# Kernel tuning notes

Hardware: AMD Instinct MI355X
Metric: run time of the kernel (lower is better)

The kernel has to match this reference:

```python
import math
import jax, jax.numpy as jnp
import numpy as np

D_MODEL = 1024
N_HEADS = 16
HEAD_DIM = D_MODEL // N_HEADS
WINDOW = 1024
BATCH = 2
SEQ = 2048


def _alibi_slopes(n_heads):
    # power-of-2 branch of ALiBiPositionalEmbedding._get_slopes
    start = 2 ** (-2 ** (-(math.log2(n_heads) - 3)))
    return jnp.asarray([start * start ** i for i in range(n_heads)], dtype=jnp.float32)


def setup_inputs() -> dict:
    key = jax.random.key(0)
    ks = jax.random.split(key, 5)
    scale = 0.02
    return {
        "x": jax.random.normal(ks[0], (BATCH, SEQ, D_MODEL), dtype=jnp.float32),
        "wq": jax.random.normal(ks[1], (D_MODEL, D_MODEL), dtype=jnp.float32) * scale,
        "bq": jnp.zeros((D_MODEL,), dtype=jnp.float32),
        "wk": jax.random.normal(ks[2], (D_MODEL, D_MODEL), dtype=jnp.float32) * scale,
        "bk": jnp.zeros((D_MODEL,), dtype=jnp.float32),
        "wv": jax.random.normal(ks[3], (D_MODEL, D_MODEL), dtype=jnp.float32) * scale,
        "bv": jnp.zeros((D_MODEL,), dtype=jnp.float32),
        "wo": jax.random.normal(ks[4], (D_MODEL, D_MODEL), dtype=jnp.float32) * scale,
        "bo": jnp.zeros((D_MODEL,), dtype=jnp.float32),
    }


def reference(x, wq, bq, wk, bk, wv, bv, wo, bo):
    B, S, _ = x.shape
    # projections (torch Linear: y = x @ W.T + b)
    q = (x @ wq.T + bq).reshape(B, S, N_HEADS, HEAD_DIM).transpose(0, 2, 1, 3)
    k = (x @ wk.T + bk).reshape(B, S, N_HEADS, HEAD_DIM).transpose(0, 2, 1, 3)
    v = (x @ wv.T + bv).reshape(B, S, N_HEADS, HEAD_DIM).transpose(0, 2, 1, 3)

    scores = jnp.einsum("bhqd,bhkd->bhqk", q, k) / math.sqrt(HEAD_DIM)

    # ALiBi bias: -|i-j| * slope_h, shape [H, S, S]
    pos = jnp.arange(S)
    slopes = _alibi_slopes(N_HEADS)  # [H]
    pos_diff = -jnp.abs(pos[None, :] - pos[:, None]).astype(scores.dtype)  # [S,S]
    scores = scores + pos_diff[None, None, :, :] * slopes[None, :, None, None]

    # causal + sliding-window mask: allow row-WINDOW < col <= row
    row = pos[:, None]
    col = pos[None, :]
    mask = (col > row) | (col <= row - WINDOW)  # [S,S] True = masked out
    neg = jnp.finfo(scores.dtype).min
    scores = jnp.where(mask[None, None, :, :], neg, scores)

    probs = jax.nn.softmax(scores, axis=-1)
    out = jnp.einsum("bhqk,bhkd->bhqd", probs, v)  # [B,H,S,D]
    out = out.transpose(0, 2, 1, 3).reshape(B, S, D_MODEL)
    return out @ wo.T + bo
```

## Files before the change

kernel.cpp:

```cpp
#include <hip/hip_runtime.h>
#include <cstdint>
#include <cstddef>

#define S_LEN 2048
#define NH 16
#define HD 64
#define DM 1024
#define WIN 1024

typedef unsigned short u16;
typedef __attribute__((ext_vector_type(8))) short bf16x8;
typedef __attribute__((ext_vector_type(4))) short bf16x4;
typedef __attribute__((ext_vector_type(4))) float f32x4;
typedef __attribute__((ext_vector_type(4))) u16 u16x4;
typedef __attribute__((ext_vector_type(2))) uint32_t u32x2;
typedef __attribute__((ext_vector_type(4))) uint32_t u32x4;

__device__ inline u16 f2b(float f) {
  union { float f; uint32_t u; } x; x.f = f;
  uint32_t r = x.u + 0x7FFFu + ((x.u >> 16) & 1u);
  return (u16)(r >> 16);
}

__device__ inline uint32_t cvt_pk_bf16(float a, float b) {
  uint32_t r;
  asm("v_cvt_pk_bf16_f32 %0, %1, %2" : "=v"(r) : "v"(a), "v"(b));
  return r;
}

__device__ inline void gload16(const void* g, void* l) {
  __builtin_amdgcn_global_load_lds((const __attribute__((address_space(1))) void*)g,
                                   (__attribute__((address_space(3))) void*)l, 16, 0, 0);
}

__global__ __launch_bounds__(256) void cvt_kernel(const float* __restrict__ src,
                                                  u16* __restrict__ dst, int n) {
  int i = (blockIdx.x * 256 + threadIdx.x) * 4;
  if (i >= n) return;
  f32x4 v = *(const f32x4*)(src + i);
  u16x4 o;
  o[0] = f2b(v[0]); o[1] = f2b(v[1]); o[2] = f2b(v[2]); o[3] = f2b(v[3]);
  *(u16x4*)(dst + i) = o;
}

__global__ __launch_bounds__(256)
void cvt4_kernel(const float* __restrict__ a, const float* __restrict__ b,
                 const float* __restrict__ c, const float* __restrict__ d,
                 u16* __restrict__ oa, u16* __restrict__ ob,
                 u16* __restrict__ oc, u16* __restrict__ od) {
  const float* src; u16* dst;
  switch (blockIdx.y) {
    case 0: src = a; dst = oa; break;
    case 1: src = b; dst = ob; break;
    case 2: src = c; dst = oc; break;
    default: src = d; dst = od; break;
  }
  int i = (blockIdx.x * 256 + threadIdx.x) * 4;
  f32x4 v = *(const f32x4*)(src + i);
  u16x4 o;
  o[0] = f2b(v[0]); o[1] = f2b(v[1]); o[2] = f2b(v[2]); o[3] = f2b(v[3]);
  *(u16x4*)(dst + i) = o;
}

template<int EPI>
__global__ __launch_bounds__(256, 4)
void gemm_nt(const u16* __restrict__ A, const u16* __restrict__ B,
             const float* __restrict__ b0, const float* __restrict__ b1,
             const float* __restrict__ b2,
             float* __restrict__ outF, u16* __restrict__ outQ,
             int M, int N, int K) {
  __shared__ u16 As[128 * 32];
  __shared__ u16 Bs[128 * 32];
  const int t = threadIdx.x;
  const int lane = t & 63, wid = t >> 6;
  const int l15 = lane & 15, l4 = lane >> 4;
  const int wr = wid >> 1, wc = wid & 1;
  const int bmB = M >> 7, bnB = N >> 7;
  const int stripe = bmB >> 3;
  const int per = stripe * bnB;
  const int job = (blockIdx.x & 7) * per + (blockIdx.x >> 3);
  const int r_ = job % per;
  const int bm = ((job / per) * stripe + r_ / bnB) << 7;
  const int bn = (r_ % bnB) << 7;
  const int srow = wid * 16 + (lane >> 2), scol = (lane & 3) * 8;
  const u16* Ag = A + (size_t)(bm + srow) * K + scol;
  const u16* Bg = B + (size_t)(bn + srow) * K + scol;
  u16* As0 = As + wid * 512;
  u16* As1 = As + 2048 + wid * 512;
  u16* Bs0 = Bs + wid * 512;
  u16* Bs1 = Bs + 2048 + wid * 512;
  const size_t rstep = (size_t)64 * K;
  f32x4 acc[4][4];
#pragma unroll
  for (int i = 0; i < 4; i++)
#pragma unroll
    for (int j = 0; j < 4; j++) acc[i][j] = (f32x4){0.f, 0.f, 0.f, 0.f};

  for (int kb = 0; kb < K; kb += 32) {
    __syncthreads();
    gload16(Ag + kb, As0);
    gload16(Ag + kb + rstep, As1);
    gload16(Bg + kb, Bs0);
    gload16(Bg + kb + rstep, Bs1);
    __syncthreads();
    bf16x8 af[4], bq[4];
#pragma unroll
    for (int mi = 0; mi < 4; mi++)
      af[mi] = *(bf16x8*)&As[(wr * 64 + mi * 16 + l15) * 32 + l4 * 8];
#pragma unroll
    for (int ni = 0; ni < 4; ni++)
      bq[ni] = *(bf16x8*)&Bs[(wc * 64 + ni * 16 + l15) * 32 + l4 * 8];
#pragma unroll
    for (int mi = 0; mi < 4; mi++)
#pragma unroll
      for (int ni = 0; ni < 4; ni++)
        acc[mi][ni] = __builtin_amdgcn_mfma_f32_16x16x32_bf16(af[mi], bq[ni], acc[mi][ni], 0, 0, 0);
  }

  const int cb = bn >> 10;
  const float* bp = (EPI == 0) ? b0 : (cb == 0 ? b0 : (cb == 1 ? b1 : b2));
#pragma unroll
  for (int mi = 0; mi < 4; mi++) {
#pragma unroll
    for (int ni = 0; ni < 4; ni++) {
#pragma unroll
      for (int r = 0; r < 4; r++) {
        int row = bm + wr * 64 + mi * 16 + l4 * 4 + r;
        int col = bn + wc * 64 + ni * 16 + l15;
        float v = acc[mi][ni][r] + bp[col & (DM - 1)];
        if (EPI == 0) {
          outF[(size_t)row * N + col] = v;
        } else {
          int b = row >> 11, s = row & (S_LEN - 1);
          int which = col >> 10, cw = col & (DM - 1);
          int h = cw >> 6, d = cw & (HD - 1);
          outQ[(size_t)which * 4194304 +
               (((size_t)(b * NH + h)) * S_LEN + s) * HD + d] = f2b(v);
        }
      }
    }
  }
}

__global__ __launch_bounds__(256)
void transpose_v(const u16* __restrict__ V, u16* __restrict__ Vt) {
  const int bh = blockIdx.y;
  const int s0 = blockIdx.x * 64;
  __shared__ u16 tile[64][72];
  const int t = threadIdx.x;
  const u16* src = V + ((size_t)bh * S_LEN + s0) * HD;
#pragma unroll
  for (int i = 0; i < 2; i++) {
    int e = t * 8 + i * 2048;
    int r = e >> 6, c = e & 63;
    *(bf16x8*)&tile[r][c] = *(const bf16x8*)(src + e);
  }
  __syncthreads();
  u16* dst = Vt + (size_t)bh * HD * S_LEN + s0;
#pragma unroll
  for (int i = 0; i < 2; i++) {
    int e = t * 8 + i * 2048;
    int d = e >> 6, s = e & 63;
    bf16x8 tmp;
#pragma unroll
    for (int j = 0; j < 8; j++) tmp[j] = (short)tile[s + j][d];
    *(bf16x8*)&dst[(size_t)d * S_LEN + s] = tmp;
  }
}

__device__ __forceinline__ void stage_tiles(const char* __restrict__ Kg,
                                            const char* __restrict__ Vg,
                                            u16* __restrict__ Kl, u16* __restrict__ Vl,
                                            int t) {
#pragma unroll
  for (int shot = 0; shot < 2; shot++) {
    int o = shot * 4096 + t * 16;
    int sw = ((o >> 7) & 7) << 4;
    gload16(Kg + (o ^ sw), (char*)Kl + o);
    gload16(Vg + (size_t)(o >> 7) * 4096 + ((o & 127) ^ sw), (char*)Vl + o);
  }
}

__device__ __forceinline__ void process_tile16(
    int kb, const u16* __restrict__ Kl, const u16* __restrict__ Vl,
    const bf16x8 qf[2], const float c16[16],
    int qw, int l15, int hi, float slope2, float qks,
    float& m, float& lsum, f32x4 O[4]) {
  const int x = l15 & 7;
  f32x4 st[4];
#pragma unroll
  for (int f = 0; f < 4; f++) st[f] = (f32x4){0.f, 0.f, 0.f, 0.f};
#pragma unroll
  for (int ks = 0; ks < 2; ks++)
#pragma unroll
    for (int f = 0; f < 4; f++) {
      bf16x8 kf = *(const bf16x8*)&Kl[(16 * f + l15) * 64 + (((4 * ks + hi) ^ x) << 3)];
      st[f] = __builtin_amdgcn_mfma_f32_16x16x32_bf16(kf, qf[ks], st[f], 0, 0, 0);
    }

  const int dkb = kb + 4 * hi - (qw + l15);
  const float base = slope2 * (float)dkb;
  const bool interior = (kb + 63 <= qw) && (kb - (qw + 15) > -WIN);
  float p[16];
  if (interior) {
#pragma unroll
    for (int f = 0; f < 4; f++)
#pragma unroll
      for (int r = 0; r < 4; r++)
        p[4 * f + r] = fmaf(st[f][r], qks, base + c16[4 * f + r]);
  } else {
#pragma unroll
    for (int f = 0; f < 4; f++)
#pragma unroll
      for (int r = 0; r < 4; r++) {
        int dk = dkb + 16 * f + r;
        float s = fmaf(st[f][r], qks, base + c16[4 * f + r]);
        p[4 * f + r] = (dk > 0 || dk <= -WIN) ? -3e38f : s;
      }
  }

  float t8[8];
#pragma unroll
  for (int r = 0; r < 8; r++) t8[r] = fmaxf(p[r], p[r + 8]);
#pragma unroll
  for (int r = 0; r < 4; r++) t8[r] = fmaxf(t8[r], t8[r + 4]);
  float rmax = fmaxf(fmaxf(t8[0], t8[1]), fmaxf(t8[2], t8[3]));
  rmax = fmaxf(rmax, __shfl_xor(rmax, 16, 64));
  rmax = fmaxf(rmax, __shfl_xor(rmax, 32, 64));

  if (!__all(rmax <= m + 8.f)) {
    float mn = fmaxf(m, rmax);
    float sc = exp2f(m - mn);
    m = mn;
    lsum *= sc;
#pragma unroll
    for (int d = 0; d < 4; d++)
#pragma unroll
      for (int r = 0; r < 4; r++) O[d][r] *= sc;
  }

#pragma unroll
  for (int r = 0; r < 16; r++) p[r] = exp2f(p[r] - m);
  float a8[8];
#pragma unroll
  for (int r = 0; r < 8; r++) a8[r] = p[r] + p[r + 8];
#pragma unroll
  for (int r = 0; r < 4; r++) a8[r] += a8[r + 4];
  lsum += (a8[0] + a8[1]) + (a8[2] + a8[3]);

  bf16x8 pb[2];
#pragma unroll
  for (int kc = 0; kc < 2; kc++) {
    u32x4 w4;
    w4[0] = cvt_pk_bf16(p[8 * kc + 0], p[8 * kc + 1]);
    w4[1] = cvt_pk_bf16(p[8 * kc + 2], p[8 * kc + 3]);
    w4[2] = cvt_pk_bf16(p[8 * kc + 4], p[8 * kc + 5]);
    w4[3] = cvt_pk_bf16(p[8 * kc + 6], p[8 * kc + 7]);
    pb[kc] = __builtin_bit_cast(bf16x8, w4);
  }

#pragma unroll
  for (int d = 0; d < 4; d++) {
#pragma unroll
    for (int kc = 0; kc < 2; kc++) {
      const int row = (16 * d + l15) * 64;
      bf16x4 a = *(const bf16x4*)&Vl[row + (((4 * kc + (hi >> 1)) ^ x) << 3) + 4 * (hi & 1)];
      bf16x4 bql = *(const bf16x4*)&Vl[row + (((4 * kc + 2 + (hi >> 1)) ^ x) << 3) + 4 * (hi & 1)];
      bf16x8 vf;
      vf[0] = a[0]; vf[1] = a[1]; vf[2] = a[2]; vf[3] = a[3];
      vf[4] = bql[0]; vf[5] = bql[1]; vf[6] = bql[2]; vf[7] = bql[3];
      O[d] = __builtin_amdgcn_mfma_f32_16x16x32_bf16(vf, pb[kc], O[d], 0, 0, 0);
    }
  }
}

__global__ __launch_bounds__(256, 4)
void attn_kernel(const u16* __restrict__ Q, const u16* __restrict__ Kg,
                 const u16* __restrict__ Vt, u16* __restrict__ attn) {
  __shared__ __align__(16) u16 Klds[2][4096];
  __shared__ __align__(16) u16 Vlds[2][4096];
  const int bid = blockIdx.x;
  const int job = (bid & 7) * 128 + (bid >> 3);
  const int bh = job >> 5;
  const int qb = ((31 - (job & 31)) + (bh << 3)) & 31;
  const int b = bh >> 4, h = bh & 15;
  const int tid = threadIdx.x;
  const int wid = tid >> 6, lane = tid & 63;
  const int l15 = lane & 15, hi = lane >> 4;
  const int q0 = qb << 6;
  const int qw = q0 + 16 * wid;
  const u16* Qp = Q + (size_t)bh * (S_LEN * HD);
  const char* Kbase = (const char*)(Kg + (size_t)bh * (S_LEN * HD));
  const char* Vbase = (const char*)(Vt + (size_t)bh * (HD * S_LEN));

  bf16x8 qf[2];
#pragma unroll
  for (int ks = 0; ks < 2; ks++)
    qf[ks] = *(const bf16x8*)(Qp + (size_t)(qw + l15) * HD + 32 * ks + 8 * hi);

  const float slope2 = exp2f(-0.5f * (float)(h + 1)) * 1.44269504f;
  const float qks = 0.125f * 1.44269504f;
  float c16[16];
#pragma unroll
  for (int f = 0; f < 4; f++)
#pragma unroll
    for (int r = 0; r < 4; r++) c16[4 * f + r] = slope2 * (float)(16 * f + r);

  float m = -1e30f, lsum = 0.f;
  f32x4 O[4];
#pragma unroll
  for (int d = 0; d < 4; d++) O[d] = (f32x4){0.f, 0.f, 0.f, 0.f};

  int lo_u = q0 - (WIN - 1); if (lo_u < 0) lo_u = 0; lo_u &= ~63;
  const int hi_u = q0;
  int lo_w = qw - (WIN - 1); if (lo_w < 0) lo_w = 0; lo_w &= ~63;
  const int last_w = (qw + 15) & ~63;

  stage_tiles(Kbase + (size_t)lo_u * 128, Vbase + (size_t)lo_u * 2,
              Klds[0], Vlds[0], tid);
  int cur = 0;
  for (int kb = lo_u; kb <= hi_u; kb += 64) {
    __syncthreads();
    if (kb + 64 <= hi_u)
      stage_tiles(Kbase + (size_t)(kb + 64) * 128, Vbase + (size_t)(kb + 64) * 2,
                  Klds[cur ^ 1], Vlds[cur ^ 1], tid);
    if (kb >= lo_w && kb <= last_w)
      process_tile16(kb, Klds[cur], Vlds[cur], qf, c16,
                     qw, l15, hi, slope2, qks, m, lsum, O);
    cur ^= 1;
  }

  lsum += __shfl_xor(lsum, 16, 64);
  lsum += __shfl_xor(lsum, 32, 64);

  const float invl = 1.f / lsum;
  u16* op = attn + ((size_t)(b * S_LEN) + qw + l15) * DM + h * HD + 4 * hi;
#pragma unroll
  for (int d = 0; d < 4; d++) {
    u32x2 w;
    w[0] = cvt_pk_bf16(O[d][0] * invl, O[d][1] * invl);
    w[1] = cvt_pk_bf16(O[d][2] * invl, O[d][3] * invl);
    *(u32x2*)(op + d * 16) = w;
  }
}

extern "C" void kernel_launch(void* const* d_in, const int* in_sizes, int n_in,
                              void* d_out, int out_size, void* d_ws, size_t ws_size,
                              hipStream_t stream) {
  const float* x  = (const float*)d_in[0];
  const float* wq = (const float*)d_in[1];
  const float* bq = (const float*)d_in[2];
  const float* wk = (const float*)d_in[3];
  const float* bk = (const float*)d_in[4];
  const float* wv = (const float*)d_in[5];
  const float* bv = (const float*)d_in[6];
  const float* wo = (const float*)d_in[7];
  const float* bo = (const float*)d_in[8];

  char* ws = (char*)d_ws;
  u16* xb    = (u16*)(ws);
  u16* wqkvb = (u16*)(ws + 8388608);
  u16* wob   = (u16*)(ws + 14680064);
  u16* QKVb  = (u16*)(ws + 16777216);
  u16* Vtb   = (u16*)(ws + 41943040);
  u16* Ab    = (u16*)(ws + 50331648);
  u16* Vb    = QKVb + 2 * 4194304;

  const int M = 4096;

  cvt_kernel<<<dim3(4096), dim3(256), 0, stream>>>(x, xb, 4194304);
  cvt4_kernel<<<dim3(1024, 4), dim3(256), 0, stream>>>(
      wq, wk, wv, wo, wqkvb, wqkvb + 1048576, wqkvb + 2097152, wob);

  gemm_nt<1><<<dim3(768), dim3(256), 0, stream>>>(xb, wqkvb, bq, bk, bv,
                                                  nullptr, QKVb, M, 3072, DM);

  transpose_v<<<dim3(32, 32), dim3(256), 0, stream>>>(Vb, Vtb);

  attn_kernel<<<dim3(1024), dim3(256), 0, stream>>>(QKVb, QKVb + 4194304, Vtb, Ab);

  gemm_nt<0><<<dim3(256), dim3(256), 0, stream>>>(Ab, wob, bo, nullptr, nullptr,
                                                  (float*)d_out, nullptr, M, DM, DM);
}
```

Measured before the change: 120.1 us.

## Split key tiles across two wave groups per attention block and merge

```diff
diff --git a/kernel.cpp b/kernel.cpp
--- a/kernel.cpp
+++ b/kernel.cpp
@@ -170,15 +170,12 @@
 
 __device__ __forceinline__ void stage_tiles(const char* __restrict__ Kg,
                                             const char* __restrict__ Vg,
-                                            u16* __restrict__ Kl, u16* __restrict__ Vl,
+                                            char* __restrict__ Kl, char* __restrict__ Vl,
                                             int t) {
-#pragma unroll
-  for (int shot = 0; shot < 2; shot++) {
-    int o = shot * 4096 + t * 16;
-    int sw = ((o >> 7) & 7) << 4;
-    gload16(Kg + (o ^ sw), (char*)Kl + o);
-    gload16(Vg + (size_t)(o >> 7) * 4096 + ((o & 127) ^ sw), (char*)Vl + o);
-  }
+  int o = t * 16;
+  int sw = ((o >> 7) & 7) << 4;
+  gload16(Kg + (o ^ sw), Kl + o);
+  gload16(Vg + (size_t)(o >> 7) * 4096 + ((o & 127) ^ sw), Vl + o);
 }
 
 __device__ __forceinline__ void process_tile16(
@@ -274,11 +271,10 @@
   }
 }
 
-__global__ __launch_bounds__(256, 4)
+__global__ __launch_bounds__(512)
 void attn_kernel(const u16* __restrict__ Q, const u16* __restrict__ Kg,
                  const u16* __restrict__ Vt, u16* __restrict__ attn) {
-  __shared__ __align__(16) u16 Klds[2][4096];
-  __shared__ __align__(16) u16 Vlds[2][4096];
+  __shared__ __align__(16) char smem[32768];
   const int bid = blockIdx.x;
   const int job = (bid & 7) * 128 + (bid >> 3);
   const int bh = job >> 5;
@@ -286,9 +282,10 @@
   const int b = bh >> 4, h = bh & 15;
   const int tid = threadIdx.x;
   const int wid = tid >> 6, lane = tid & 63;
+  const int rg = wid & 3, split = wid >> 2;
   const int l15 = lane & 15, hi = lane >> 4;
   const int q0 = qb << 6;
-  const int qw = q0 + 16 * wid;
+  const int qw = q0 + 16 * rg;
   const u16* Qp = Q + (size_t)bh * (S_LEN * HD);
   const char* Kbase = (const char*)(Kg + (size_t)bh * (S_LEN * HD));
   const char* Vbase = (const char*)(Vt + (size_t)bh * (HD * S_LEN));
@@ -313,34 +310,57 @@
 
   int lo_u = q0 - (WIN - 1); if (lo_u < 0) lo_u = 0; lo_u &= ~63;
   const int hi_u = q0;
-  int lo_w = qw - (WIN - 1); if (lo_w < 0) lo_w = 0; lo_w &= ~63;
-  const int last_w = (qw + 15) & ~63;
 
   stage_tiles(Kbase + (size_t)lo_u * 128, Vbase + (size_t)lo_u * 2,
-              Klds[0], Vlds[0], tid);
+              smem, smem + 16384, tid);
   int cur = 0;
   for (int kb = lo_u; kb <= hi_u; kb += 64) {
     __syncthreads();
     if (kb + 64 <= hi_u)
       stage_tiles(Kbase + (size_t)(kb + 64) * 128, Vbase + (size_t)(kb + 64) * 2,
-                  Klds[cur ^ 1], Vlds[cur ^ 1], tid);
-    if (kb >= lo_w && kb <= last_w)
-      process_tile16(kb, Klds[cur], Vlds[cur], qf, c16,
+                  smem + (cur ^ 1) * 8192, smem + 16384 + (cur ^ 1) * 8192, tid);
+    if ((((kb - lo_u) >> 6) & 1) == split)
+      process_tile16(kb, (const u16*)(smem + cur * 8192),
+                     (const u16*)(smem + 16384 + cur * 8192), qf, c16,
                      qw, l15, hi, slope2, qks, m, lsum, O);
     cur ^= 1;
   }
 
-  lsum += __shfl_xor(lsum, 16, 64);
-  lsum += __shfl_xor(lsum, 32, 64);
-
-  const float invl = 1.f / lsum;
-  u16* op = attn + ((size_t)(b * S_LEN) + qw + l15) * DM + h * HD + 4 * hi;
-#pragma unroll
-  for (int d = 0; d < 4; d++) {
-    u32x2 w;
-    w[0] = cvt_pk_bf16(O[d][0] * invl, O[d][1] * invl);
-    w[1] = cvt_pk_bf16(O[d][2] * invl, O[d][3] * invl);
-    *(u32x2*)(op + d * 16) = w;
+  __syncthreads();
+  float* comb = (float*)smem;
+  if (wid >= 4) {
+    float* c = comb + ((size_t)rg * 64 + lane) * 18;
+#pragma unroll
+    for (int d = 0; d < 4; d++)
+#pragma unroll
+      for (int r = 0; r < 4; r++) c[4 * d + r] = O[d][r];
+    c[16] = m; c[17] = lsum;
+  }
+  __syncthreads();
+  if (wid < 4) {
+    const float* c = comb + ((size_t)wid * 64 + lane) * 18;
+    float m1 = c[16], l1 = c[17];
+    float M = fmaxf(m, m1);
+    float w0 = exp2f(m - M), w1 = exp2f(m1 - M);
+    lsum = lsum * w0 + l1 * w1;
+#pragma unroll
+    for (int d = 0; d < 4; d++)
+#pragma unroll
+      for (int r = 0; r < 4; r++)
+        O[d][r] = O[d][r] * w0 + c[4 * d + r] * w1;
+
+    lsum += __shfl_xor(lsum, 16, 64);
+    lsum += __shfl_xor(lsum, 32, 64);
+
+    const float invl = 1.f / lsum;
+    u16* op = attn + ((size_t)(b * S_LEN) + qw + l15) * DM + h * HD + 4 * hi;
+#pragma unroll
+    for (int d = 0; d < 4; d++) {
+      u32x2 w;
+      w[0] = cvt_pk_bf16(O[d][0] * invl, O[d][1] * invl);
+      w[1] = cvt_pk_bf16(O[d][2] * invl, O[d][3] * invl);
+      *(u32x2*)(op + d * 16) = w;
+    }
   }
 }
 
@@ -377,7 +397,7 @@
 
   transpose_v<<<dim3(32, 32), dim3(256), 0, stream>>>(Vb, Vtb);
 
-  attn_kernel<<<dim3(1024), dim3(256), 0, stream>>>(QKVb, QKVb + 4194304, Vtb, Ab);
+  attn_kernel<<<dim3(1024), dim3(512), 0, stream>>>(QKVb, QKVb + 4194304, Vtb, Ab);
 
   gemm_nt<0><<<dim3(256), dim3(256), 0, stream>>>(Ab, wob, bo, nullptr, nullptr,
                                                   (float*)d_out, nullptr, M, DM, DM);
```

After: 127.6 us. +6.2%, slower.

## Pre-pack K/V into MFMA fragment layout and run single-wave attention blocks

Applied to the files above, without the earlier changes.

```diff
diff --git a/kernel.cpp b/kernel.cpp
--- a/kernel.cpp
+++ b/kernel.cpp
@@ -168,130 +168,66 @@
   }
 }
 
-__device__ __forceinline__ void stage_tiles(const char* __restrict__ Kg,
-                                            const char* __restrict__ Vg,
-                                            u16* __restrict__ Kl, u16* __restrict__ Vl,
-                                            int t) {
+__global__ __launch_bounds__(256)
+void repack_frags(const u16* __restrict__ Krow, const u16* __restrict__ Vt,
+                  u16* __restrict__ Kf, u16* __restrict__ Vf) {
+  __shared__ __align__(16) u16 Kl[4096];
+  __shared__ __align__(16) u16 Vl[4096];
+  const int T = blockIdx.x, bh = blockIdx.y;
+  const int tid = threadIdx.x;
+  const int wid = tid >> 6, lane = tid & 63;
+  const int l15 = lane & 15, hi = lane >> 4;
+  const char* Kg = (const char*)(Krow + (size_t)bh * (S_LEN * HD)) + (size_t)(T * 64) * 128;
+  const char* Vg = (const char*)(Vt + (size_t)bh * (HD * S_LEN)) + (size_t)(T * 64) * 2;
 #pragma unroll
   for (int shot = 0; shot < 2; shot++) {
-    int o = shot * 4096 + t * 16;
+    int o = shot * 4096 + tid * 16;
     int sw = ((o >> 7) & 7) << 4;
     gload16(Kg + (o ^ sw), (char*)Kl + o);
     gload16(Vg + (size_t)(o >> 7) * 4096 + ((o & 127) ^ sw), (char*)Vl + o);
   }
-}
-
-__device__ __forceinline__ void process_tile16(
-    int kb, const u16* __restrict__ Kl, const u16* __restrict__ Vl,
-    const bf16x8 qf[2], const float c16[16],
-    int qw, int l15, int hi, float slope2, float qks,
-    float& m, float& lsum, f32x4 O[4]) {
+  __syncthreads();
   const int x = l15 & 7;
-  f32x4 st[4];
-#pragma unroll
-  for (int f = 0; f < 4; f++) st[f] = (f32x4){0.f, 0.f, 0.f, 0.f};
-#pragma unroll
-  for (int ks = 0; ks < 2; ks++)
-#pragma unroll
-    for (int f = 0; f < 4; f++) {
-      bf16x8 kf = *(const bf16x8*)&Kl[(16 * f + l15) * 64 + (((4 * ks + hi) ^ x) << 3)];
-      st[f] = __builtin_amdgcn_mfma_f32_16x16x32_bf16(kf, qf[ks], st[f], 0, 0, 0);
-    }
-
-  const int dkb = kb + 4 * hi - (qw + l15);
-  const float base = slope2 * (float)dkb;
-  const bool interior = (kb + 63 <= qw) && (kb - (qw + 15) > -WIN);
-  float p[16];
-  if (interior) {
-#pragma unroll
-    for (int f = 0; f < 4; f++)
-#pragma unroll
-      for (int r = 0; r < 4; r++)
-        p[4 * f + r] = fmaf(st[f][r], qks, base + c16[4 * f + r]);
-  } else {
-#pragma unroll
-    for (int f = 0; f < 4; f++)
-#pragma unroll
-      for (int r = 0; r < 4; r++) {
-        int dk = dkb + 16 * f + r;
-        float s = fmaf(st[f][r], qks, base + c16[4 * f + r]);
-        p[4 * f + r] = (dk > 0 || dk <= -WIN) ? -3e38f : s;
+  if (wid == 0) {
+    u16* kd = Kf + ((size_t)bh * 32 + T) * 4096 + lane * 8;
+#pragma unroll
+    for (int ks = 0; ks < 2; ks++)
+#pragma unroll
+      for (int f = 0; f < 4; f++) {
+        bf16x8 kfr = *(const bf16x8*)&Kl[(16 * f + l15) * 64 + (((4 * ks + hi) ^ x) << 3)];
+        *(bf16x8*)(kd + (ks * 4 + f) * 512) = kfr;
       }
-  }
-
-  float t8[8];
-#pragma unroll
-  for (int r = 0; r < 8; r++) t8[r] = fmaxf(p[r], p[r + 8]);
-#pragma unroll
-  for (int r = 0; r < 4; r++) t8[r] = fmaxf(t8[r], t8[r + 4]);
-  float rmax = fmaxf(fmaxf(t8[0], t8[1]), fmaxf(t8[2], t8[3]));
-  rmax = fmaxf(rmax, __shfl_xor(rmax, 16, 64));
-  rmax = fmaxf(rmax, __shfl_xor(rmax, 32, 64));
-
-  if (!__all(rmax <= m + 8.f)) {
-    float mn = fmaxf(m, rmax);
-    float sc = exp2f(m - mn);
-    m = mn;
-    lsum *= sc;
+  } else if (wid == 1) {
+    u16* vd = Vf + ((size_t)bh * 32 + T) * 4096 + lane * 8;
 #pragma unroll
     for (int d = 0; d < 4; d++)
 #pragma unroll
-      for (int r = 0; r < 4; r++) O[d][r] *= sc;
-  }
-
-#pragma unroll
-  for (int r = 0; r < 16; r++) p[r] = exp2f(p[r] - m);
-  float a8[8];
-#pragma unroll
-  for (int r = 0; r < 8; r++) a8[r] = p[r] + p[r + 8];
-#pragma unroll
-  for (int r = 0; r < 4; r++) a8[r] += a8[r + 4];
-  lsum += (a8[0] + a8[1]) + (a8[2] + a8[3]);
-
-  bf16x8 pb[2];
-#pragma unroll
-  for (int kc = 0; kc < 2; kc++) {
-    u32x4 w4;
-    w4[0] = cvt_pk_bf16(p[8 * kc + 0], p[8 * kc + 1]);
-    w4[1] = cvt_pk_bf16(p[8 * kc + 2], p[8 * kc + 3]);
-    w4[2] = cvt_pk_bf16(p[8 * kc + 4], p[8 * kc + 5]);
-    w4[3] = cvt_pk_bf16(p[8 * kc + 6], p[8 * kc + 7]);
-    pb[kc] = __builtin_bit_cast(bf16x8, w4);
-  }
-
-#pragma unroll
-  for (int d = 0; d < 4; d++) {
-#pragma unroll
-    for (int kc = 0; kc < 2; kc++) {
-      const int row = (16 * d + l15) * 64;
-      bf16x4 a = *(const bf16x4*)&Vl[row + (((4 * kc + (hi >> 1)) ^ x) << 3) + 4 * (hi & 1)];
-      bf16x4 bql = *(const bf16x4*)&Vl[row + (((4 * kc + 2 + (hi >> 1)) ^ x) << 3) + 4 * (hi & 1)];
-      bf16x8 vf;
-      vf[0] = a[0]; vf[1] = a[1]; vf[2] = a[2]; vf[3] = a[3];
-      vf[4] = bql[0]; vf[5] = bql[1]; vf[6] = bql[2]; vf[7] = bql[3];
-      O[d] = __builtin_amdgcn_mfma_f32_16x16x32_bf16(vf, pb[kc], O[d], 0, 0, 0);
-    }
-  }
-}
-
-__global__ __launch_bounds__(256, 4)
-void attn_kernel(const u16* __restrict__ Q, const u16* __restrict__ Kg,
-                 const u16* __restrict__ Vt, u16* __restrict__ attn) {
-  __shared__ __align__(16) u16 Klds[2][4096];
-  __shared__ __align__(16) u16 Vlds[2][4096];
+      for (int kc = 0; kc < 2; kc++) {
+        const int row = (16 * d + l15) * 64;
+        bf16x4 a = *(const bf16x4*)&Vl[row + (((4 * kc + (hi >> 1)) ^ x) << 3) + 4 * (hi & 1)];
+        bf16x4 bq2 = *(const bf16x4*)&Vl[row + (((4 * kc + 2 + (hi >> 1)) ^ x) << 3) + 4 * (hi & 1)];
+        bf16x8 vfr;
+        vfr[0] = a[0]; vfr[1] = a[1]; vfr[2] = a[2]; vfr[3] = a[3];
+        vfr[4] = bq2[0]; vfr[5] = bq2[1]; vfr[6] = bq2[2]; vfr[7] = bq2[3];
+        *(bf16x8*)(vd + (d * 2 + kc) * 512) = vfr;
+      }
+  }
+}
+
+__global__ __launch_bounds__(64)
+void attn_kernel(const u16* __restrict__ Q, const u16* __restrict__ Kf,
+                 const u16* __restrict__ Vf, u16* __restrict__ attn) {
   const int bid = blockIdx.x;
-  const int job = (bid & 7) * 128 + (bid >> 3);
-  const int bh = job >> 5;
-  const int qb = ((31 - (job & 31)) + (bh << 3)) & 31;
+  const int job = (bid & 7) * 512 + (bid >> 3);
+  const int bh = job >> 7;
+  const int qt = ((127 - (job & 127)) + (bh << 3)) & 127;
   const int b = bh >> 4, h = bh & 15;
-  const int tid = threadIdx.x;
-  const int wid = tid >> 6, lane = tid & 63;
+  const int lane = threadIdx.x;
   const int l15 = lane & 15, hi = lane >> 4;
-  const int q0 = qb << 6;
-  const int qw = q0 + 16 * wid;
+  const int qw = qt << 4;
   const u16* Qp = Q + (size_t)bh * (S_LEN * HD);
-  const char* Kbase = (const char*)(Kg + (size_t)bh * (S_LEN * HD));
-  const char* Vbase = (const char*)(Vt + (size_t)bh * (HD * S_LEN));
+  const u16* Kfb = Kf + (size_t)bh * 131072 + lane * 8;
+  const u16* Vfb = Vf + (size_t)bh * 131072 + lane * 8;
 
   bf16x8 qf[2];
 #pragma unroll
@@ -311,23 +247,99 @@
 #pragma unroll
   for (int d = 0; d < 4; d++) O[d] = (f32x4){0.f, 0.f, 0.f, 0.f};
 
-  int lo_u = q0 - (WIN - 1); if (lo_u < 0) lo_u = 0; lo_u &= ~63;
-  const int hi_u = q0;
-  int lo_w = qw - (WIN - 1); if (lo_w < 0) lo_w = 0; lo_w &= ~63;
-  const int last_w = (qw + 15) & ~63;
-
-  stage_tiles(Kbase + (size_t)lo_u * 128, Vbase + (size_t)lo_u * 2,
-              Klds[0], Vlds[0], tid);
-  int cur = 0;
-  for (int kb = lo_u; kb <= hi_u; kb += 64) {
-    __syncthreads();
-    if (kb + 64 <= hi_u)
-      stage_tiles(Kbase + (size_t)(kb + 64) * 128, Vbase + (size_t)(kb + 64) * 2,
-                  Klds[cur ^ 1], Vlds[cur ^ 1], tid);
-    if (kb >= lo_w && kb <= last_w)
-      process_tile16(kb, Klds[cur], Vlds[cur], qf, c16,
-                     qw, l15, hi, slope2, qks, m, lsum, O);
-    cur ^= 1;
+  int lo = qw - (WIN - 1); if (lo < 0) lo = 0; lo &= ~63;
+  const int last = (qw + 15) & ~63;
+
+  for (int kb = lo; kb <= last; kb += 64) {
+    const u16* kp = Kfb + (size_t)(kb >> 6) * 4096;
+    const u16* vp = Vfb + (size_t)(kb >> 6) * 4096;
+    bf16x8 kfr[2][4], vfr[4][2];
+#pragma unroll
+    for (int ks = 0; ks < 2; ks++)
+#pragma unroll
+      for (int f = 0; f < 4; f++)
+        kfr[ks][f] = *(const bf16x8*)(kp + (ks * 4 + f) * 512);
+#pragma unroll
+    for (int d = 0; d < 4; d++)
+#pragma unroll
+      for (int kc = 0; kc < 2; kc++)
+        vfr[d][kc] = *(const bf16x8*)(vp + (d * 2 + kc) * 512);
+
+    f32x4 st[4];
+#pragma unroll
+    for (int f = 0; f < 4; f++) st[f] = (f32x4){0.f, 0.f, 0.f, 0.f};
+#pragma unroll
+    for (int ks = 0; ks < 2; ks++)
+#pragma unroll
+      for (int f = 0; f < 4; f++)
+        st[f] = __builtin_amdgcn_mfma_f32_16x16x32_bf16(kfr[ks][f], qf[ks], st[f], 0, 0, 0);
+
+    const int dkb = kb + 4 * hi - (qw + l15);
+    const float base = slope2 * (float)dkb;
+    const bool interior = (kb + 63 <= qw) && (kb - (qw + 15) > -WIN);
+    float p[16];
+    if (interior) {
+#pragma unroll
+      for (int f = 0; f < 4; f++)
+#pragma unroll
+        for (int r = 0; r < 4; r++)
+          p[4 * f + r] = fmaf(st[f][r], qks, base + c16[4 * f + r]);
+    } else {
+#pragma unroll
+      for (int f = 0; f < 4; f++)
+#pragma unroll
+        for (int r = 0; r < 4; r++) {
+          int dk = dkb + 16 * f + r;
+          float s = fmaf(st[f][r], qks, base + c16[4 * f + r]);
+          p[4 * f + r] = (dk > 0 || dk <= -WIN) ? -3e38f : s;
+        }
+    }
+
+    float t8[8];
+#pragma unroll
+    for (int r = 0; r < 8; r++) t8[r] = fmaxf(p[r], p[r + 8]);
+#pragma unroll
+    for (int r = 0; r < 4; r++) t8[r] = fmaxf(t8[r], t8[r + 4]);
+    float rmax = fmaxf(fmaxf(t8[0], t8[1]), fmaxf(t8[2], t8[3]));
+    rmax = fmaxf(rmax, __shfl_xor(rmax, 16, 64));
+    rmax = fmaxf(rmax, __shfl_xor(rmax, 32, 64));
+
+    if (!__all(rmax <= m + 8.f)) {
+      float mn = fmaxf(m, rmax);
+      float sc = exp2f(m - mn);
+      m = mn;
+      lsum *= sc;
+#pragma unroll
+      for (int d = 0; d < 4; d++)
+#pragma unroll
+        for (int r = 0; r < 4; r++) O[d][r] *= sc;
+    }
+
+#pragma unroll
+    for (int r = 0; r < 16; r++) p[r] = exp2f(p[r] - m);
+    float a8[8];
+#pragma unroll
+    for (int r = 0; r < 8; r++) a8[r] = p[r] + p[r + 8];
+#pragma unroll
+    for (int r = 0; r < 4; r++) a8[r] += a8[r + 4];
+    lsum += (a8[0] + a8[1]) + (a8[2] + a8[3]);
+
+    bf16x8 pb[2];
+#pragma unroll
+    for (int kc = 0; kc < 2; kc++) {
+      u32x4 w4;
+      w4[0] = cvt_pk_bf16(p[8 * kc + 0], p[8 * kc + 1]);
+      w4[1] = cvt_pk_bf16(p[8 * kc + 2], p[8 * kc + 3]);
+      w4[2] = cvt_pk_bf16(p[8 * kc + 4], p[8 * kc + 5]);
+      w4[3] = cvt_pk_bf16(p[8 * kc + 6], p[8 * kc + 7]);
+      pb[kc] = __builtin_bit_cast(bf16x8, w4);
+    }
+
+#pragma unroll
+    for (int d = 0; d < 4; d++)
+#pragma unroll
+      for (int kc = 0; kc < 2; kc++)
+        O[d] = __builtin_amdgcn_mfma_f32_16x16x32_bf16(vfr[d][kc], pb[kc], O[d], 0, 0, 0);
   }
 
   lsum += __shfl_xor(lsum, 16, 64);
@@ -359,12 +371,14 @@
 
   char* ws = (char*)d_ws;
   u16* xb    = (u16*)(ws);
+  u16* Kfb   = (u16*)(ws);
   u16* wqkvb = (u16*)(ws + 8388608);
   u16* wob   = (u16*)(ws + 14680064);
   u16* QKVb  = (u16*)(ws + 16777216);
   u16* Vtb   = (u16*)(ws + 41943040);
   u16* Ab    = (u16*)(ws + 50331648);
   u16* Vb    = QKVb + 2 * 4194304;
+  u16* Vfb   = Vb;
 
   const int M = 4096;
 
@@ -377,7 +391,9 @@
 
   transpose_v<<<dim3(32, 32), dim3(256), 0, stream>>>(Vb, Vtb);
 
-  attn_kernel<<<dim3(1024), dim3(256), 0, stream>>>(QKVb, QKVb + 4194304, Vtb, Ab);
+  repack_frags<<<dim3(32, 32), dim3(256), 0, stream>>>(QKVb + 4194304, Vtb, Kfb, Vfb);
+
+  attn_kernel<<<dim3(4096), dim3(64), 0, stream>>>(QKVb, Kfb, Vfb, Ab);
 
   gemm_nt<0><<<dim3(256), dim3(256), 0, stream>>>(Ab, wob, bo, nullptr, nullptr,
                                                   (float*)d_out, nullptr, M, DM, DM);
```

Measured after the change: 128.4 us. 6.9% more time.
